# Kernel tuning notes

Measured on AMD Instinct MI355X. Metric: run time of the kernel, lower is better.

Reference implementation:

```python
import jax, jax.numpy as jnp
import numpy as np

C_IN = 256
K = 4
C_QK = C_IN // K  # 64


def setup_inputs() -> dict:
    key = jax.random.key(0)
    ks = jax.random.split(key, 9)
    B, C, H, W = 4, C_IN, 64, 64
    s = 0.02
    return {
        "x": jax.random.normal(ks[0], (B, C, H, W), dtype=jnp.float32),
        # 1x1 convs stored as dense [out, in] matrices (kernel_size=1)
        "wq": jax.random.normal(ks[1], (C_QK, C), dtype=jnp.float32) * s,
        "bq": jax.random.normal(ks[2], (C_QK,), dtype=jnp.float32) * s,
        "wk": jax.random.normal(ks[3], (C_QK, C), dtype=jnp.float32) * s,
        "bk": jax.random.normal(ks[4], (C_QK,), dtype=jnp.float32) * s,
        "wv": jax.random.normal(ks[5], (C, C), dtype=jnp.float32) * s,
        "bv": jax.random.normal(ks[6], (C,), dtype=jnp.float32) * s,
        "wg": jax.random.normal(ks[7], (C, C), dtype=jnp.float32) * s,
        "bg": jax.random.normal(ks[8], (C,), dtype=jnp.float32) * s,
    }


def reference(x, wq, bq, wk, bk, wv, bv, wg, bg):
    B, C, H, W = x.shape
    N = H * W
    xf = x.reshape(B, C, N)  # [B, C, N]
    # 1x1 conv == per-pixel linear over channels
    q = jnp.einsum("oc,bcn->bon", wq, xf) + bq[None, :, None]  # [B, Cqk, N]
    k = jnp.einsum("oc,bcn->bon", wk, xf) + bk[None, :, None]  # [B, Cqk, N]
    v = jnp.einsum("oc,bcn->bon", wv, xf) + bv[None, :, None]  # [B, C, N]
    # energy[b, n, m] = <q[:, n], k[:, m]>  (n = query pos, m = key pos)
    energy = jnp.einsum("bon,bom->bnm", q, k)  # [B, N, N]
    energy = jax.nn.elu(energy) / N
    # out[b, c, m] = sum_n v[b, c, n] * energy[b, n, m]
    out = jnp.einsum("bcn,bnm->bcm", v, energy).reshape(B, C, H, W)
    out = jnp.einsum("oc,bchw->bohw", wg, out) + bg[None, :, None, None]
    return out
```

## Files before the change

kernel.cpp:

```cpp
#include <hip/hip_runtime.h>

#define B_ 4
#define C_ 256
#define CQK 64
#define N_ 4096
#define SEG 2
#define SEGN (N_ / SEG)
#define NB 128
#define ITERS (SEGN / NB)
#define TS 512

typedef _Float16 f16;
typedef __attribute__((ext_vector_type(8))) _Float16 f16x8;
typedef __attribute__((ext_vector_type(4))) _Float16 f16x4;
typedef __attribute__((ext_vector_type(4))) float f32x4;
typedef __attribute__((ext_vector_type(4))) float float4v;

#define TILE_OFF(l15, quad) ((l15) * 32 + (quad) * 8)

__global__ __launch_bounds__(256) void prep_w(
    const float* __restrict__ wq, const float* __restrict__ wk,
    const float* __restrict__ wv, const float* __restrict__ wg,
    f16* __restrict__ WQt, f16* __restrict__ WKt, f16* __restrict__ WVt,
    f16* __restrict__ WGt) {
  int chunk = blockIdx.x * 256 + threadIdx.x;
  if (chunk >= 20480) return;
  const float* src;
  f16* dst;
  int lo;
  if (chunk < 2048) { src = wq; dst = WQt; lo = chunk * 8; }
  else if (chunk < 4096) { src = wk; dst = WKt; lo = (chunk - 2048) * 8; }
  else if (chunk < 12288) { src = wv; dst = WVt; lo = (chunk - 4096) * 8; }
  else { src = wg; dst = WGt; lo = (chunk - 12288) * 8; }
  int o = lo >> 8, k = lo & 255;
  f16x8 v;
#pragma unroll
  for (int j = 0; j < 8; j++) v[j] = (f16)src[lo + j];
  *(f16x8*)(dst + ((size_t)(o >> 4) * 8 + (k >> 5)) * TS + (o & 15) * 32 + (k & 31)) = v;
}

__global__ __launch_bounds__(256) void proj(
    const float* __restrict__ x, const f16* __restrict__ WQt,
    const f16* __restrict__ WKt, const f16* __restrict__ WVt,
    const float* __restrict__ bq, const float* __restrict__ bk,
    const float* __restrict__ bv, f16* __restrict__ QTt, f16* __restrict__ KTt,
    f16* __restrict__ Vt) {
  __shared__ float xs[32][265];
  __shared__ f16 xt[2 * 8 * TS];
  int n0 = blockIdx.x * 32;
  int b = blockIdx.y;
  int tid = threadIdx.x, lane = tid & 63, w = tid >> 6;
  int l15 = lane & 15, quad = lane >> 4;
  const float* xb = x + (size_t)b * C_ * N_;

#pragma unroll
  for (int i = 0; i < 8; i++) {
    int c = i * 32 + (tid >> 3);
    int n4 = (tid & 7) * 4;
    float4v f4 = *(const float4v*)(xb + (size_t)c * N_ + n0 + n4);
#pragma unroll
    for (int j = 0; j < 4; j++) xs[n4 + j][c] = f4[j];
  }
  __syncthreads();
#pragma unroll
  for (int i = 0; i < 4; i++) {
    int t = w + i * 4;
    int nt = t >> 3, kt = t & 7;
    f16x8 v;
#pragma unroll
    for (int j = 0; j < 8; j++)
      v[j] = (f16)xs[nt * 16 + l15][kt * 32 + quad * 8 + j];
    *(f16x8*)(xt + (nt * 8 + kt) * TS + l15 * 32 + quad * 8) = v;
  }
  __syncthreads();

  f32x4 acc[6][2];
#pragma unroll
  for (int j = 0; j < 6; j++)
#pragma unroll
    for (int nt = 0; nt < 2; nt++) acc[j][nt] = (f32x4){0.f, 0.f, 0.f, 0.f};

#pragma unroll
  for (int kt = 0; kt < 8; kt++) {
    f16x8 xf[2];
#pragma unroll
    for (int nt = 0; nt < 2; nt++)
      xf[nt] = *(const f16x8*)(xt + (nt * 8 + kt) * TS + TILE_OFF(l15, quad));
#pragma unroll
    for (int j = 0; j < 6; j++) {
      int g = w * 6 + j;
      const f16* Wt;
      int ot;
      bool isV = g < 16;
      if (isV) { Wt = WVt; ot = g; }
      else if (g < 20) { Wt = WQt; ot = g - 16; }
      else { Wt = WKt; ot = g - 20; }
      f16x8 wf = *(const f16x8*)(Wt + ((size_t)ot * 8 + kt) * TS + TILE_OFF(l15, quad));
#pragma unroll
      for (int nt = 0; nt < 2; nt++)
        acc[j][nt] = isV
            ? __builtin_amdgcn_mfma_f32_16x16x32_f16(xf[nt], wf, acc[j][nt], 0, 0, 0)
            : __builtin_amdgcn_mfma_f32_16x16x32_f16(wf, xf[nt], acc[j][nt], 0, 0, 0);
    }
  }

  f16* vbout = Vt + (size_t)b * C_ * N_;
#pragma unroll
  for (int j = 0; j < 6; j++) {
    int g = w * 6 + j;
    if (g < 16) {
      float bvv = bv[16 * g + l15];
#pragma unroll
      for (int nt = 0; nt < 2; nt++) {
        f16x4 vals;
#pragma unroll
        for (int r = 0; r < 4; r++) vals[r] = (f16)(acc[j][nt][r] + bvv);
        *(f16x4*)(vbout + ((size_t)g * 128 + (n0 >> 5)) * TS +
                  l15 * 32 + 16 * nt + 4 * quad) = vals;
      }
    } else {
      int oq = (g < 20) ? (g - 16) : (g - 20);
      const float* bias = (g < 20) ? bq : bk;
      f16* ob = ((g < 20) ? QTt : KTt) + (size_t)b * N_ * CQK;
#pragma unroll
      for (int nt = 0; nt < 2; nt++) {
        f16x4 vals;
#pragma unroll
        for (int r = 0; r < 4; r++)
          vals[r] = (f16)(acc[j][nt][r] + bias[16 * oq + 4 * quad + r]);
        *(f16x4*)(ob + (((size_t)(n0 >> 4) + nt) * 2 + (oq >> 1)) * TS + l15 * 32 +
                  16 * (oq & 1) + 4 * quad) = vals;
      }
    }
  }
}

__global__ __launch_bounds__(256, 2) void attn(const f16* __restrict__ qt,
                                               const f16* __restrict__ kt,
                                               const f16* __restrict__ v,
                                               const f16* __restrict__ WGt,
                                               f16* __restrict__ part) {
  __shared__ __align__(16) f16 sPt[2][64][128];
  int sb = blockIdx.x;
  int seg = sb >> 2;
  int b = sb & 3;
  int m0 = blockIdx.y * 64;
  int tid = threadIdx.x, lane = tid & 63, w = tid >> 6;
  int l15 = lane & 15, quad = lane >> 4;
  const f16* qtb = qt + (size_t)b * N_ * CQK;
  const f16* ktb = kt + (size_t)b * N_ * CQK;
  const f16* vb = v + (size_t)b * C_ * N_;

  f32x4 oacc[4][4];
#pragma unroll
  for (int ct = 0; ct < 4; ct++)
#pragma unroll
    for (int mt = 0; mt < 4; mt++) oacc[ct][mt] = (f32x4){0.f, 0.f, 0.f, 0.f};

  f16x8 kf[4][2];
#pragma unroll
  for (int mt = 0; mt < 4; mt++)
#pragma unroll
    for (int ks = 0; ks < 2; ks++)
      kf[mt][ks] = *(const f16x8*)(ktb + ((size_t)((m0 >> 4) + mt) * 2 + ks) * TS +
                                   TILE_OFF(l15, quad));

  f16x8 qf[2][2];
#pragma unroll
  for (int nt = 0; nt < 2; nt++)
#pragma unroll
    for (int ks = 0; ks < 2; ks++)
      qf[nt][ks] = *(const f16x8*)(qtb +
                                   ((size_t)(((seg * SEGN) >> 4) + 2 * w + nt) * 2 + ks) * TS +
                                   TILE_OFF(l15, quad));

  {
    char* buf = (char*)sPt[0];
#pragma unroll
    for (int nt = 0; nt < 2; nt++) {
      f32x4 sacc[4];
#pragma unroll
      for (int mt = 0; mt < 4; mt++) sacc[mt] = (f32x4){0.f, 0.f, 0.f, 0.f};
#pragma unroll
      for (int ks = 0; ks < 2; ks++)
#pragma unroll
        for (int mt = 0; mt < 4; mt++)
          sacc[mt] = __builtin_amdgcn_mfma_f32_16x16x32_f16(qf[nt][ks], kf[mt][ks],
                                                            sacc[mt], 0, 0, 0);
#pragma unroll
      for (int mt = 0; mt < 4; mt++) {
        f16x4 p;
#pragma unroll
        for (int r = 0; r < 4; r++) {
          float s = sacc[mt][r];
          p[r] = (f16)(s > 0.0f ? s : (__expf(s) - 1.0f));
        }
        int row = 16 * mt + l15;
        int colb = (64 * w + 32 * nt + 8 * quad) ^ ((row & 7) << 4);
        *(f16x4*)(buf + row * 256 + colb) = p;
      }
    }
  }
  {
    int nq = seg * SEGN + NB;
#pragma unroll
    for (int nt = 0; nt < 2; nt++)
#pragma unroll
      for (int ks = 0; ks < 2; ks++)
        qf[nt][ks] = *(const f16x8*)(qtb +
                                     ((size_t)((nq >> 4) + 2 * w + nt) * 2 + ks) * TS +
                                     TILE_OFF(l15, quad));
  }
  __syncthreads();

  for (int it = 0; it < ITERS; it++) {
    int n0 = seg * SEGN + it * NB;
    char* rbuf = (char*)sPt[it & 1];
    char* wbuf = (char*)sPt[(it + 1) & 1];
    bool hasNext = (it + 1 < ITERS);

    f16x8 vfA[2][4];
#pragma unroll
    for (int ks = 0; ks < 2; ks++)
#pragma unroll
      for (int ct = 0; ct < 4; ct++)
        vfA[ks][ct] = *(const f16x8*)(vb +
                                      ((size_t)(4 * w + ct) * 128 + (n0 >> 5) + ks) * TS +
                                      TILE_OFF(l15, quad));

    f32x4 s0[4], s1[4];
    if (hasNext) {
#pragma unroll
      for (int mt = 0; mt < 4; mt++) s0[mt] = (f32x4){0.f, 0.f, 0.f, 0.f};
#pragma unroll
      for (int ks = 0; ks < 2; ks++)
#pragma unroll
        for (int mt = 0; mt < 4; mt++)
          s0[mt] = __builtin_amdgcn_mfma_f32_16x16x32_f16(qf[0][ks], kf[mt][ks],
                                                          s0[mt], 0, 0, 0);
    }

    f16x8 pa[4];
#pragma unroll
    for (int mt = 0; mt < 4; mt++) {
      int row = 16 * mt + l15;
      pa[mt] = *(const f16x8*)(rbuf + row * 256 + ((quad * 16) ^ ((row & 7) << 4)));
    }
#pragma unroll
    for (int ct = 0; ct < 4; ct++)
#pragma unroll
      for (int mt = 0; mt < 4; mt++)
        oacc[ct][mt] = __builtin_amdgcn_mfma_f32_16x16x32_f16(vfA[0][ct], pa[mt],
                                                              oacc[ct][mt], 0, 0, 0);

    f16x8 vfB[2][4];
#pragma unroll
    for (int ks = 0; ks < 2; ks++)
#pragma unroll
      for (int ct = 0; ct < 4; ct++)
        vfB[ks][ct] = *(const f16x8*)(vb + ((size_t)(4 * w + ct) * 128 + (n0 >> 5) +
                                            2 + ks) * TS +
                                      TILE_OFF(l15, quad));

    if (hasNext) {
#pragma unroll
      for (int mt = 0; mt < 4; mt++) {
        f16x4 p;
#pragma unroll
        for (int r = 0; r < 4; r++) {
          float s = s0[mt][r];
          p[r] = (f16)(s > 0.0f ? s : (__expf(s) - 1.0f));
        }
        int row = 16 * mt + l15;
        int colb = (64 * w + 8 * quad) ^ ((row & 7) << 4);
        *(f16x4*)(wbuf + row * 256 + colb) = p;
      }
    }

#pragma unroll
    for (int mt = 0; mt < 4; mt++) {
      int row = 16 * mt + l15;
      pa[mt] = *(const f16x8*)(rbuf + row * 256 + ((64 + quad * 16) ^ ((row & 7) << 4)));
    }
#pragma unroll
    for (int ct = 0; ct < 4; ct++)
#pragma unroll
      for (int mt = 0; mt < 4; mt++)
        oacc[ct][mt] = __builtin_amdgcn_mfma_f32_16x16x32_f16(vfA[1][ct], pa[mt],
                                                              oacc[ct][mt], 0, 0, 0);

    if (hasNext) {
#pragma unroll
      for (int mt = 0; mt < 4; mt++) s1[mt] = (f32x4){0.f, 0.f, 0.f, 0.f};
#pragma unroll
      for (int ks = 0; ks < 2; ks++)
#pragma unroll
        for (int mt = 0; mt < 4; mt++)
          s1[mt] = __builtin_amdgcn_mfma_f32_16x16x32_f16(qf[1][ks], kf[mt][ks],
                                                          s1[mt], 0, 0, 0);
    }

#pragma unroll
    for (int mt = 0; mt < 4; mt++) {
      int row = 16 * mt + l15;
      pa[mt] = *(const f16x8*)(rbuf + row * 256 + ((128 + quad * 16) ^ ((row & 7) << 4)));
    }
#pragma unroll
    for (int ct = 0; ct < 4; ct++)
#pragma unroll
      for (int mt = 0; mt < 4; mt++)
        oacc[ct][mt] = __builtin_amdgcn_mfma_f32_16x16x32_f16(vfB[0][ct], pa[mt],
                                                              oacc[ct][mt], 0, 0, 0);

    if (hasNext) {
#pragma unroll
      for (int mt = 0; mt < 4; mt++) {
        f16x4 p;
#pragma unroll
        for (int r = 0; r < 4; r++) {
          float s = s1[mt][r];
          p[r] = (f16)(s > 0.0f ? s : (__expf(s) - 1.0f));
        }
        int row = 16 * mt + l15;
        int colb = (64 * w + 32 + 8 * quad) ^ ((row & 7) << 4);
        *(f16x4*)(wbuf + row * 256 + colb) = p;
      }
      if (it + 2 < ITERS) {
        int nq = seg * SEGN + (it + 2) * NB;
#pragma unroll
        for (int nt = 0; nt < 2; nt++)
#pragma unroll
          for (int ks = 0; ks < 2; ks++)
            qf[nt][ks] = *(const f16x8*)(qtb +
                                         ((size_t)((nq >> 4) + 2 * w + nt) * 2 + ks) * TS +
                                         TILE_OFF(l15, quad));
      }
    }

#pragma unroll
    for (int mt = 0; mt < 4; mt++) {
      int row = 16 * mt + l15;
      pa[mt] = *(const f16x8*)(rbuf + row * 256 + ((192 + quad * 16) ^ ((row & 7) << 4)));
    }
#pragma unroll
    for (int ct = 0; ct < 4; ct++)
#pragma unroll
      for (int mt = 0; mt < 4; mt++)
        oacc[ct][mt] = __builtin_amdgcn_mfma_f32_16x16x32_f16(vfB[1][ct], pa[mt],
                                                              oacc[ct][mt], 0, 0, 0);

    __syncthreads();
  }

  f16* obuf = (f16*)sPt;
#pragma unroll
  for (int ct = 0; ct < 4; ct++) {
#pragma unroll
    for (int mt = 0; mt < 4; mt++) {
      f16x4 vals;
#pragma unroll
      for (int r = 0; r < 4; r++)
        vals[r] = (f16)(oacc[ct][mt][r] * (1.0f / (float)N_));
      *(f16x4*)(obuf + (mt * 8 + 2 * w + (ct >> 1)) * TS + l15 * 32 +
                16 * (ct & 1) + 4 * quad) = vals;
    }
  }
  __syncthreads();
  f32x4 accO[4][4];
#pragma unroll
  for (int ot = 0; ot < 4; ot++)
#pragma unroll
    for (int mt = 0; mt < 4; mt++) accO[ot][mt] = (f32x4){0.f, 0.f, 0.f, 0.f};
#pragma unroll
  for (int kt = 0; kt < 8; kt++) {
    f16x8 bO[4];
#pragma unroll
    for (int mt = 0; mt < 4; mt++)
      bO[mt] = *(const f16x8*)(obuf + (mt * 8 + kt) * TS + TILE_OFF(l15, quad));
#pragma unroll
    for (int ot = 0; ot < 4; ot++) {
      f16x8 af = *(const f16x8*)(WGt + ((size_t)(4 * w + ot) * 8 + kt) * TS +
                                 TILE_OFF(l15, quad));
#pragma unroll
      for (int mt = 0; mt < 4; mt++)
        accO[ot][mt] = __builtin_amdgcn_mfma_f32_16x16x32_f16(af, bO[mt], accO[ot][mt], 0, 0, 0);
    }
  }
  f16* pb = part + ((size_t)(seg * B_ + b) * C_) * N_;
#pragma unroll
  for (int ot = 0; ot < 4; ot++) {
#pragma unroll
    for (int mt = 0; mt < 4; mt++) {
      int m = m0 + 16 * mt + l15;
#pragma unroll
      for (int r = 0; r < 4; r++) {
        int o = 64 * w + 16 * ot + 4 * quad + r;
        pb[(size_t)o * N_ + m] = (f16)accO[ot][mt][r];
      }
    }
  }
}

__global__ __launch_bounds__(256) void combine(const f16* __restrict__ part,
                                               const float* __restrict__ bg,
                                               float* __restrict__ out) {
  size_t i = ((size_t)blockIdx.x * 256 + threadIdx.x) * 8;
  f16x8 p0 = *(const f16x8*)(part + i);
  f16x8 p1 = *(const f16x8*)(part + (size_t)B_ * C_ * N_ + i);
  float bgo = bg[(i >> 12) & 255];
  float4v r0, r1;
#pragma unroll
  for (int j = 0; j < 4; j++) r0[j] = (float)p0[j] + (float)p1[j] + bgo;
#pragma unroll
  for (int j = 0; j < 4; j++) r1[j] = (float)p0[4 + j] + (float)p1[4 + j] + bgo;
  *(float4v*)(out + i) = r0;
  *(float4v*)(out + i + 4) = r1;
}

extern "C" void kernel_launch(void* const* d_in, const int* in_sizes, int n_in,
                              void* d_out, int out_size, void* d_ws, size_t ws_size,
                              hipStream_t stream) {
  const float* x = (const float*)d_in[0];
  const float* wq = (const float*)d_in[1];
  const float* bq = (const float*)d_in[2];
  const float* wk = (const float*)d_in[3];
  const float* bk = (const float*)d_in[4];
  const float* wv = (const float*)d_in[5];
  const float* bv = (const float*)d_in[6];
  const float* wg = (const float*)d_in[7];
  const float* bg = (const float*)d_in[8];
  float* out = (float*)d_out;

  char* ws = (char*)d_ws;
  f16* QTt = (f16*)ws; ws += (size_t)B_ * N_ * CQK * sizeof(f16);
  f16* KTt = (f16*)ws; ws += (size_t)B_ * N_ * CQK * sizeof(f16);
  f16* Vt  = (f16*)ws; ws += (size_t)B_ * C_ * N_ * sizeof(f16);
  f16* WQt = (f16*)ws; ws += (size_t)CQK * C_ * sizeof(f16);
  f16* WKt = (f16*)ws; ws += (size_t)CQK * C_ * sizeof(f16);
  f16* WVt = (f16*)ws; ws += (size_t)C_ * C_ * sizeof(f16);
  f16* WGt = (f16*)ws; ws += (size_t)C_ * C_ * sizeof(f16);
  f16* PART = (f16*)ws; ws += (size_t)SEG * B_ * C_ * N_ * sizeof(f16);

  prep_w<<<dim3(80), 256, 0, stream>>>(wq, wk, wv, wg, WQt, WKt, WVt, WGt);
  proj<<<dim3(N_ / 32, B_), 256, 0, stream>>>(x, WQt, WKt, WVt, bq, bk, bv,
                                              QTt, KTt, Vt);
  attn<<<dim3(SEG * B_, N_ / 64), 256, 0, stream>>>(QTt, KTt, Vt, WGt, PART);
  combine<<<dim3(2048), 256, 0, stream>>>(PART, bg, out);
}
```

Baseline: 161.0 us.

## Fuse four kernels into one persistent kernel with software grid barriers

```diff
diff --git a/kernel.cpp b/kernel.cpp
--- a/kernel.cpp
+++ b/kernel.cpp
@@ -9,6 +9,7 @@
 #define NB 128
 #define ITERS (SEGN / NB)
 #define TS 512
+#define NBLK 512
 
 typedef _Float16 f16;
 typedef __attribute__((ext_vector_type(8))) _Float16 f16x8;
@@ -18,403 +19,425 @@
 
 #define TILE_OFF(l15, quad) ((l15) * 32 + (quad) * 8)
 
-__global__ __launch_bounds__(256) void prep_w(
-    const float* __restrict__ wq, const float* __restrict__ wk,
-    const float* __restrict__ wv, const float* __restrict__ wg,
-    f16* __restrict__ WQt, f16* __restrict__ WKt, f16* __restrict__ WVt,
-    f16* __restrict__ WGt) {
-  int chunk = blockIdx.x * 256 + threadIdx.x;
-  if (chunk >= 20480) return;
-  const float* src;
-  f16* dst;
-  int lo;
-  if (chunk < 2048) { src = wq; dst = WQt; lo = chunk * 8; }
-  else if (chunk < 4096) { src = wk; dst = WKt; lo = (chunk - 2048) * 8; }
-  else if (chunk < 12288) { src = wv; dst = WVt; lo = (chunk - 4096) * 8; }
-  else { src = wg; dst = WGt; lo = (chunk - 12288) * 8; }
-  int o = lo >> 8, k = lo & 255;
-  f16x8 v;
-#pragma unroll
-  for (int j = 0; j < 8; j++) v[j] = (f16)src[lo + j];
-  *(f16x8*)(dst + ((size_t)(o >> 4) * 8 + (k >> 5)) * TS + (o & 15) * 32 + (k & 31)) = v;
+__device__ __forceinline__ void gridbar(unsigned* bar) {
+  __syncthreads();
+  if (threadIdx.x == 0) {
+    __threadfence();
+    unsigned gen = __hip_atomic_load(bar + 1, __ATOMIC_RELAXED, __HIP_MEMORY_SCOPE_AGENT);
+    unsigned old = atomicAdd(bar, 1u);
+    if (old == NBLK - 1) {
+      __hip_atomic_store(bar, 0u, __ATOMIC_RELAXED, __HIP_MEMORY_SCOPE_AGENT);
+      __hip_atomic_fetch_add(bar + 1, 1u, __ATOMIC_RELEASE, __HIP_MEMORY_SCOPE_AGENT);
+    } else {
+      while (__hip_atomic_load(bar + 1, __ATOMIC_ACQUIRE, __HIP_MEMORY_SCOPE_AGENT) == gen)
+        __builtin_amdgcn_s_sleep(2);
+    }
+    __threadfence();
+  }
+  __syncthreads();
 }
 
-__global__ __launch_bounds__(256) void proj(
-    const float* __restrict__ x, const f16* __restrict__ WQt,
-    const f16* __restrict__ WKt, const f16* __restrict__ WVt,
-    const float* __restrict__ bq, const float* __restrict__ bk,
-    const float* __restrict__ bv, f16* __restrict__ QTt, f16* __restrict__ KTt,
-    f16* __restrict__ Vt) {
-  __shared__ float xs[32][265];
-  __shared__ f16 xt[2 * 8 * TS];
-  int n0 = blockIdx.x * 32;
-  int b = blockIdx.y;
+__global__ __launch_bounds__(256, 2) void fused(
+    const float* __restrict__ x, const float* __restrict__ wq,
+    const float* __restrict__ bq, const float* __restrict__ wk,
+    const float* __restrict__ bk, const float* __restrict__ wv,
+    const float* __restrict__ bv, const float* __restrict__ wg,
+    const float* __restrict__ bg, f16* __restrict__ QTt, f16* __restrict__ KTt,
+    f16* __restrict__ Vt, f16* __restrict__ WQt, f16* __restrict__ WKt,
+    f16* __restrict__ WVt, f16* __restrict__ WGt, f16* __restrict__ part,
+    float* __restrict__ out, unsigned* __restrict__ bar) {
+  __shared__ __align__(16) union {
+    struct { float xs[32][265]; f16 xt[2 * 8 * TS]; } p;
+    f16 sPt[2][64][128];
+  } sh;
+  int bid = blockIdx.x;
   int tid = threadIdx.x, lane = tid & 63, w = tid >> 6;
   int l15 = lane & 15, quad = lane >> 4;
-  const float* xb = x + (size_t)b * C_ * N_;
-
-#pragma unroll
-  for (int i = 0; i < 8; i++) {
-    int c = i * 32 + (tid >> 3);
-    int n4 = (tid & 7) * 4;
-    float4v f4 = *(const float4v*)(xb + (size_t)c * N_ + n0 + n4);
-#pragma unroll
-    for (int j = 0; j < 4; j++) xs[n4 + j][c] = f4[j];
+
+  {
+    int chunk = bid * 256 + tid;
+    if (chunk < 20480) {
+      const float* src;
+      f16* dst;
+      int lo;
+      if (chunk < 2048) { src = wq; dst = WQt; lo = chunk * 8; }
+      else if (chunk < 4096) { src = wk; dst = WKt; lo = (chunk - 2048) * 8; }
+      else if (chunk < 12288) { src = wv; dst = WVt; lo = (chunk - 4096) * 8; }
+      else { src = wg; dst = WGt; lo = (chunk - 12288) * 8; }
+      int o = lo >> 8, k = lo & 255;
+      f16x8 v;
+#pragma unroll
+      for (int j = 0; j < 8; j++) v[j] = (f16)src[lo + j];
+      *(f16x8*)(dst + ((size_t)(o >> 4) * 8 + (k >> 5)) * TS + (o & 15) * 32 +
+                (k & 31)) = v;
+    }
   }
-  __syncthreads();
-#pragma unroll
-  for (int i = 0; i < 4; i++) {
-    int t = w + i * 4;
-    int nt = t >> 3, kt = t & 7;
-    f16x8 v;
-#pragma unroll
-    for (int j = 0; j < 8; j++)
-      v[j] = (f16)xs[nt * 16 + l15][kt * 32 + quad * 8 + j];
-    *(f16x8*)(xt + (nt * 8 + kt) * TS + l15 * 32 + quad * 8) = v;
-  }
-  __syncthreads();
-
-  f32x4 acc[6][2];
-#pragma unroll
-  for (int j = 0; j < 6; j++)
-#pragma unroll
-    for (int nt = 0; nt < 2; nt++) acc[j][nt] = (f32x4){0.f, 0.f, 0.f, 0.f};
-
-#pragma unroll
-  for (int kt = 0; kt < 8; kt++) {
-    f16x8 xf[2];
-#pragma unroll
-    for (int nt = 0; nt < 2; nt++)
-      xf[nt] = *(const f16x8*)(xt + (nt * 8 + kt) * TS + TILE_OFF(l15, quad));
+  gridbar(bar);
+
+  {
+    int n0 = (bid & 127) * 32;
+    int b = bid >> 7;
+    const float* xb = x + (size_t)b * C_ * N_;
+
+#pragma unroll
+    for (int i = 0; i < 8; i++) {
+      int c = i * 32 + (tid >> 3);
+      int n4 = (tid & 7) * 4;
+      float4v f4 = *(const float4v*)(xb + (size_t)c * N_ + n0 + n4);
+#pragma unroll
+      for (int j = 0; j < 4; j++) sh.p.xs[n4 + j][c] = f4[j];
+    }
+    __syncthreads();
+#pragma unroll
+    for (int i = 0; i < 4; i++) {
+      int t = w + i * 4;
+      int nt = t >> 3, kt = t & 7;
+      f16x8 v;
+#pragma unroll
+      for (int j = 0; j < 8; j++)
+        v[j] = (f16)sh.p.xs[nt * 16 + l15][kt * 32 + quad * 8 + j];
+      *(f16x8*)(sh.p.xt + (nt * 8 + kt) * TS + l15 * 32 + quad * 8) = v;
+    }
+    __syncthreads();
+
+    f32x4 acc[6][2];
+#pragma unroll
+    for (int j = 0; j < 6; j++)
+#pragma unroll
+      for (int nt = 0; nt < 2; nt++) acc[j][nt] = (f32x4){0.f, 0.f, 0.f, 0.f};
+
+#pragma unroll
+    for (int kt = 0; kt < 8; kt++) {
+      f16x8 xf[2];
+#pragma unroll
+      for (int nt = 0; nt < 2; nt++)
+        xf[nt] = *(const f16x8*)(sh.p.xt + (nt * 8 + kt) * TS + TILE_OFF(l15, quad));
+#pragma unroll
+      for (int j = 0; j < 6; j++) {
+        int g = w * 6 + j;
+        const f16* Wt;
+        int ot;
+        bool isV = g < 16;
+        if (isV) { Wt = WVt; ot = g; }
+        else if (g < 20) { Wt = WQt; ot = g - 16; }
+        else { Wt = WKt; ot = g - 20; }
+        f16x8 wf = *(const f16x8*)(Wt + ((size_t)ot * 8 + kt) * TS + TILE_OFF(l15, quad));
+#pragma unroll
+        for (int nt = 0; nt < 2; nt++)
+          acc[j][nt] = isV
+              ? __builtin_amdgcn_mfma_f32_16x16x32_f16(xf[nt], wf, acc[j][nt], 0, 0, 0)
+              : __builtin_amdgcn_mfma_f32_16x16x32_f16(wf, xf[nt], acc[j][nt], 0, 0, 0);
+      }
+    }
+
+    f16* vbout = Vt + (size_t)b * C_ * N_;
 #pragma unroll
     for (int j = 0; j < 6; j++) {
       int g = w * 6 + j;
-      const f16* Wt;
-      int ot;
-      bool isV = g < 16;
-      if (isV) { Wt = WVt; ot = g; }
-      else if (g < 20) { Wt = WQt; ot = g - 16; }
-      else { Wt = WKt; ot = g - 20; }
-      f16x8 wf = *(const f16x8*)(Wt + ((size_t)ot * 8 + kt) * TS + TILE_OFF(l15, quad));
-#pragma unroll
-      for (int nt = 0; nt < 2; nt++)
-        acc[j][nt] = isV
-            ? __builtin_amdgcn_mfma_f32_16x16x32_f16(xf[nt], wf, acc[j][nt], 0, 0, 0)
-            : __builtin_amdgcn_mfma_f32_16x16x32_f16(wf, xf[nt], acc[j][nt], 0, 0, 0);
+      if (g < 16) {
+        float bvv = bv[16 * g + l15];
+#pragma unroll
+        for (int nt = 0; nt < 2; nt++) {
+          f16x4 vals;
+#pragma unroll
+          for (int r = 0; r < 4; r++) vals[r] = (f16)(acc[j][nt][r] + bvv);
+          *(f16x4*)(vbout + ((size_t)g * 128 + (n0 >> 5)) * TS +
+                    l15 * 32 + 16 * nt + 4 * quad) = vals;
+        }
+      } else {
+        int oq = (g < 20) ? (g - 16) : (g - 20);
+        const float* bias = (g < 20) ? bq : bk;
+        f16* ob = ((g < 20) ? QTt : KTt) + (size_t)b * N_ * CQK;
+#pragma unroll
+        for (int nt = 0; nt < 2; nt++) {
+          f16x4 vals;
+#pragma unroll
+          for (int r = 0; r < 4; r++)
+            vals[r] = (f16)(acc[j][nt][r] + bias[16 * oq + 4 * quad + r]);
+          *(f16x4*)(ob + (((size_t)(n0 >> 4) + nt) * 2 + (oq >> 1)) * TS + l15 * 32 +
+                    16 * (oq & 1) + 4 * quad) = vals;
+        }
+      }
     }
   }
-
-  f16* vbout = Vt + (size_t)b * C_ * N_;
-#pragma unroll
-  for (int j = 0; j < 6; j++) {
-    int g = w * 6 + j;
-    if (g < 16) {
-      float bvv = bv[16 * g + l15];
-#pragma unroll
-      for (int nt = 0; nt < 2; nt++) {
-        f16x4 vals;
-#pragma unroll
-        for (int r = 0; r < 4; r++) vals[r] = (f16)(acc[j][nt][r] + bvv);
-        *(f16x4*)(vbout + ((size_t)g * 128 + (n0 >> 5)) * TS +
-                  l15 * 32 + 16 * nt + 4 * quad) = vals;
-      }
-    } else {
-      int oq = (g < 20) ? (g - 16) : (g - 20);
-      const float* bias = (g < 20) ? bq : bk;
-      f16* ob = ((g < 20) ? QTt : KTt) + (size_t)b * N_ * CQK;
-#pragma unroll
-      for (int nt = 0; nt < 2; nt++) {
-        f16x4 vals;
-#pragma unroll
-        for (int r = 0; r < 4; r++)
-          vals[r] = (f16)(acc[j][nt][r] + bias[16 * oq + 4 * quad + r]);
-        *(f16x4*)(ob + (((size_t)(n0 >> 4) + nt) * 2 + (oq >> 1)) * TS + l15 * 32 +
-                  16 * (oq & 1) + 4 * quad) = vals;
-      }
-    }
-  }
-}
-
-__global__ __launch_bounds__(256, 2) void attn(const f16* __restrict__ qt,
-                                               const f16* __restrict__ kt,
-                                               const f16* __restrict__ v,
-                                               const f16* __restrict__ WGt,
-                                               f16* __restrict__ part) {
-  __shared__ __align__(16) f16 sPt[2][64][128];
-  int sb = blockIdx.x;
-  int seg = sb >> 2;
-  int b = sb & 3;
-  int m0 = blockIdx.y * 64;
-  int tid = threadIdx.x, lane = tid & 63, w = tid >> 6;
-  int l15 = lane & 15, quad = lane >> 4;
-  const f16* qtb = qt + (size_t)b * N_ * CQK;
-  const f16* ktb = kt + (size_t)b * N_ * CQK;
-  const f16* vb = v + (size_t)b * C_ * N_;
-
-  f32x4 oacc[4][4];
-#pragma unroll
-  for (int ct = 0; ct < 4; ct++)
-#pragma unroll
-    for (int mt = 0; mt < 4; mt++) oacc[ct][mt] = (f32x4){0.f, 0.f, 0.f, 0.f};
-
-  f16x8 kf[4][2];
-#pragma unroll
-  for (int mt = 0; mt < 4; mt++)
-#pragma unroll
-    for (int ks = 0; ks < 2; ks++)
-      kf[mt][ks] = *(const f16x8*)(ktb + ((size_t)((m0 >> 4) + mt) * 2 + ks) * TS +
-                                   TILE_OFF(l15, quad));
-
-  f16x8 qf[2][2];
-#pragma unroll
-  for (int nt = 0; nt < 2; nt++)
-#pragma unroll
-    for (int ks = 0; ks < 2; ks++)
-      qf[nt][ks] = *(const f16x8*)(qtb +
-                                   ((size_t)(((seg * SEGN) >> 4) + 2 * w + nt) * 2 + ks) * TS +
-                                   TILE_OFF(l15, quad));
+  gridbar(bar);
 
   {
-    char* buf = (char*)sPt[0];
-#pragma unroll
-    for (int nt = 0; nt < 2; nt++) {
-      f32x4 sacc[4];
-#pragma unroll
-      for (int mt = 0; mt < 4; mt++) sacc[mt] = (f32x4){0.f, 0.f, 0.f, 0.f};
+    int sb = bid & 7;
+    int seg = sb >> 2;
+    int b = sb & 3;
+    int m0 = (bid >> 3) * 64;
+    const f16* qtb = QTt + (size_t)b * N_ * CQK;
+    const f16* ktb = KTt + (size_t)b * N_ * CQK;
+    const f16* vb = Vt + (size_t)b * C_ * N_;
+
+    f32x4 oacc[4][4];
+#pragma unroll
+    for (int ct = 0; ct < 4; ct++)
+#pragma unroll
+      for (int mt = 0; mt < 4; mt++) oacc[ct][mt] = (f32x4){0.f, 0.f, 0.f, 0.f};
+
+    f16x8 kf[4][2];
+#pragma unroll
+    for (int mt = 0; mt < 4; mt++)
 #pragma unroll
       for (int ks = 0; ks < 2; ks++)
-#pragma unroll
-        for (int mt = 0; mt < 4; mt++)
-          sacc[mt] = __builtin_amdgcn_mfma_f32_16x16x32_f16(qf[nt][ks], kf[mt][ks],
-                                                            sacc[mt], 0, 0, 0);
-#pragma unroll
-      for (int mt = 0; mt < 4; mt++) {
-        f16x4 p;
-#pragma unroll
-        for (int r = 0; r < 4; r++) {
-          float s = sacc[mt][r];
-          p[r] = (f16)(s > 0.0f ? s : (__expf(s) - 1.0f));
-        }
-        int row = 16 * mt + l15;
-        int colb = (64 * w + 32 * nt + 8 * quad) ^ ((row & 7) << 4);
-        *(f16x4*)(buf + row * 256 + colb) = p;
-      }
-    }
-  }
-  {
-    int nq = seg * SEGN + NB;
+        kf[mt][ks] = *(const f16x8*)(ktb + ((size_t)((m0 >> 4) + mt) * 2 + ks) * TS +
+                                     TILE_OFF(l15, quad));
+
+    f16x8 qf[2][2];
 #pragma unroll
     for (int nt = 0; nt < 2; nt++)
 #pragma unroll
       for (int ks = 0; ks < 2; ks++)
         qf[nt][ks] = *(const f16x8*)(qtb +
-                                     ((size_t)((nq >> 4) + 2 * w + nt) * 2 + ks) * TS +
+                                     ((size_t)(((seg * SEGN) >> 4) + 2 * w + nt) * 2 + ks) * TS +
                                      TILE_OFF(l15, quad));
+
+    {
+      char* buf = (char*)sh.sPt[0];
+#pragma unroll
+      for (int nt = 0; nt < 2; nt++) {
+        f32x4 sacc[4];
+#pragma unroll
+        for (int mt = 0; mt < 4; mt++) sacc[mt] = (f32x4){0.f, 0.f, 0.f, 0.f};
+#pragma unroll
+        for (int ks = 0; ks < 2; ks++)
+#pragma unroll
+          for (int mt = 0; mt < 4; mt++)
+            sacc[mt] = __builtin_amdgcn_mfma_f32_16x16x32_f16(qf[nt][ks], kf[mt][ks],
+                                                              sacc[mt], 0, 0, 0);
+#pragma unroll
+        for (int mt = 0; mt < 4; mt++) {
+          f16x4 p;
+#pragma unroll
+          for (int r = 0; r < 4; r++) {
+            float s = sacc[mt][r];
+            p[r] = (f16)(s > 0.0f ? s : (__expf(s) - 1.0f));
+          }
+          int row = 16 * mt + l15;
+          int colb = (64 * w + 32 * nt + 8 * quad) ^ ((row & 7) << 4);
+          *(f16x4*)(buf + row * 256 + colb) = p;
+        }
+      }
+    }
+    {
+      int nq = seg * SEGN + NB;
+#pragma unroll
+      for (int nt = 0; nt < 2; nt++)
+#pragma unroll
+        for (int ks = 0; ks < 2; ks++)
+          qf[nt][ks] = *(const f16x8*)(qtb +
+                                       ((size_t)((nq >> 4) + 2 * w + nt) * 2 + ks) * TS +
+                                       TILE_OFF(l15, quad));
+    }
+    __syncthreads();
+
+    for (int it = 0; it < ITERS; it++) {
+      int n0 = seg * SEGN + it * NB;
+      char* rbuf = (char*)sh.sPt[it & 1];
+      char* wbuf = (char*)sh.sPt[(it + 1) & 1];
+      bool hasNext = (it + 1 < ITERS);
+
+      f16x8 vfA[2][4];
+#pragma unroll
+      for (int ks = 0; ks < 2; ks++)
+#pragma unroll
+        for (int ct = 0; ct < 4; ct++)
+          vfA[ks][ct] = *(const f16x8*)(vb +
+                                        ((size_t)(4 * w + ct) * 128 + (n0 >> 5) + ks) * TS +
+                                        TILE_OFF(l15, quad));
+
+      f32x4 s0[4], s1[4];
+      if (hasNext) {
+#pragma unroll
+        for (int mt = 0; mt < 4; mt++) s0[mt] = (f32x4){0.f, 0.f, 0.f, 0.f};
+#pragma unroll
+        for (int ks = 0; ks < 2; ks++)
+#pragma unroll
+          for (int mt = 0; mt < 4; mt++)
+            s0[mt] = __builtin_amdgcn_mfma_f32_16x16x32_f16(qf[0][ks], kf[mt][ks],
+                                                            s0[mt], 0, 0, 0);
+      }
+
+      f16x8 pa[4];
+#pragma unroll
+      for (int mt = 0; mt < 4; mt++) {
+        int row = 16 * mt + l15;
+        pa[mt] = *(const f16x8*)(rbuf + row * 256 + ((quad * 16) ^ ((row & 7) << 4)));
+      }
+#pragma unroll
+      for (int ct = 0; ct < 4; ct++)
+#pragma unroll
+        for (int mt = 0; mt < 4; mt++)
+          oacc[ct][mt] = __builtin_amdgcn_mfma_f32_16x16x32_f16(vfA[0][ct], pa[mt],
+                                                                oacc[ct][mt], 0, 0, 0);
+
+      f16x8 vfB[2][4];
+#pragma unroll
+      for (int ks = 0; ks < 2; ks++)
+#pragma unroll
+        for (int ct = 0; ct < 4; ct++)
+          vfB[ks][ct] = *(const f16x8*)(vb + ((size_t)(4 * w + ct) * 128 + (n0 >> 5) +
+                                              2 + ks) * TS +
+                                        TILE_OFF(l15, quad));
+
+      if (hasNext) {
+#pragma unroll
+        for (int mt = 0; mt < 4; mt++) {
+          f16x4 p;
+#pragma unroll
+          for (int r = 0; r < 4; r++) {
+            float s = s0[mt][r];
+            p[r] = (f16)(s > 0.0f ? s : (__expf(s) - 1.0f));
+          }
+          int row = 16 * mt + l15;
+          int colb = (64 * w + 8 * quad) ^ ((row & 7) << 4);
+          *(f16x4*)(wbuf + row * 256 + colb) = p;
+        }
+      }
+
+#pragma unroll
+      for (int mt = 0; mt < 4; mt++) {
+        int row = 16 * mt + l15;
+        pa[mt] = *(const f16x8*)(rbuf + row * 256 + ((64 + quad * 16) ^ ((row & 7) << 4)));
+      }
+#pragma unroll
+      for (int ct = 0; ct < 4; ct++)
+#pragma unroll
+        for (int mt = 0; mt < 4; mt++)
+          oacc[ct][mt] = __builtin_amdgcn_mfma_f32_16x16x32_f16(vfA[1][ct], pa[mt],
+                                                                oacc[ct][mt], 0, 0, 0);
+
+      if (hasNext) {
+#pragma unroll
+        for (int mt = 0; mt < 4; mt++) s1[mt] = (f32x4){0.f, 0.f, 0.f, 0.f};
+#pragma unroll
+        for (int ks = 0; ks < 2; ks++)
+#pragma unroll
+          for (int mt = 0; mt < 4; mt++)
+            s1[mt] = __builtin_amdgcn_mfma_f32_16x16x32_f16(qf[1][ks], kf[mt][ks],
+                                                            s1[mt], 0, 0, 0);
+      }
+
+#pragma unroll
+      for (int mt = 0; mt < 4; mt++) {
+        int row = 16 * mt + l15;
+        pa[mt] = *(const f16x8*)(rbuf + row * 256 + ((128 + quad * 16) ^ ((row & 7) << 4)));
+      }
+#pragma unroll
+      for (int ct = 0; ct < 4; ct++)
+#pragma unroll
+        for (int mt = 0; mt < 4; mt++)
+          oacc[ct][mt] = __builtin_amdgcn_mfma_f32_16x16x32_f16(vfB[0][ct], pa[mt],
+                                                                oacc[ct][mt], 0, 0, 0);
+
+      if (hasNext) {
+#pragma unroll
+        for (int mt = 0; mt < 4; mt++) {
+          f16x4 p;
+#pragma unroll
+          for (int r = 0; r < 4; r++) {
+            float s = s1[mt][r];
+            p[r] = (f16)(s > 0.0f ? s : (__expf(s) - 1.0f));
+          }
+          int row = 16 * mt + l15;
+          int colb = (64 * w + 32 + 8 * quad) ^ ((row & 7) << 4);
+          *(f16x4*)(wbuf + row * 256 + colb) = p;
+        }
+        if (it + 2 < ITERS) {
+          int nq = seg * SEGN + (it + 2) * NB;
+#pragma unroll
+          for (int nt = 0; nt < 2; nt++)
+#pragma unroll
+            for (int ks = 0; ks < 2; ks++)
+              qf[nt][ks] = *(const f16x8*)(qtb +
+                                           ((size_t)((nq >> 4) + 2 * w + nt) * 2 + ks) * TS +
+                                           TILE_OFF(l15, quad));
+        }
+      }
+
+#pragma unroll
+      for (int mt = 0; mt < 4; mt++) {
+        int row = 16 * mt + l15;
+        pa[mt] = *(const f16x8*)(rbuf + row * 256 + ((192 + quad * 16) ^ ((row & 7) << 4)));
+      }
+#pragma unroll
+      for (int ct = 0; ct < 4; ct++)
+#pragma unroll
+        for (int mt = 0; mt < 4; mt++)
+          oacc[ct][mt] = __builtin_amdgcn_mfma_f32_16x16x32_f16(vfB[1][ct], pa[mt],
+                                                                oacc[ct][mt], 0, 0, 0);
+
+      __syncthreads();
+    }
+
+    f16* obuf = (f16*)sh.sPt;
+#pragma unroll
+    for (int ct = 0; ct < 4; ct++) {
+#pragma unroll
+      for (int mt = 0; mt < 4; mt++) {
+        f16x4 vals;
+#pragma unroll
+        for (int r = 0; r < 4; r++)
+          vals[r] = (f16)(oacc[ct][mt][r] * (1.0f / (float)N_));
+        *(f16x4*)(obuf + (mt * 8 + 2 * w + (ct >> 1)) * TS + l15 * 32 +
+                  16 * (ct & 1) + 4 * quad) = vals;
+      }
+    }
+    __syncthreads();
+    f32x4 accO[4][4];
+#pragma unroll
+    for (int ot = 0; ot < 4; ot++)
+#pragma unroll
+      for (int mt = 0; mt < 4; mt++) accO[ot][mt] = (f32x4){0.f, 0.f, 0.f, 0.f};
+#pragma unroll
+    for (int kt = 0; kt < 8; kt++) {
+      f16x8 bO[4];
+#pragma unroll
+      for (int mt = 0; mt < 4; mt++)
+        bO[mt] = *(const f16x8*)(obuf + (mt * 8 + kt) * TS + TILE_OFF(l15, quad));
+#pragma unroll
+      for (int ot = 0; ot < 4; ot++) {
+        f16x8 af = *(const f16x8*)(WGt + ((size_t)(4 * w + ot) * 8 + kt) * TS +
+                                   TILE_OFF(l15, quad));
+#pragma unroll
+        for (int mt = 0; mt < 4; mt++)
+          accO[ot][mt] = __builtin_amdgcn_mfma_f32_16x16x32_f16(af, bO[mt], accO[ot][mt],
+                                                                0, 0, 0);
+      }
+    }
+    f16* pb = part + ((size_t)(seg * B_ + b) * C_) * N_;
+#pragma unroll
+    for (int ot = 0; ot < 4; ot++) {
+#pragma unroll
+      for (int mt = 0; mt < 4; mt++) {
+        int m = m0 + 16 * mt + l15;
+#pragma unroll
+        for (int r = 0; r < 4; r++) {
+          int o = 64 * w + 16 * ot + 4 * quad + r;
+          pb[(size_t)o * N_ + m] = (f16)accO[ot][mt][r];
+        }
+      }
+    }
   }
-  __syncthreads();
-
-  for (int it = 0; it < ITERS; it++) {
-    int n0 = seg * SEGN + it * NB;
-    char* rbuf = (char*)sPt[it & 1];
-    char* wbuf = (char*)sPt[(it + 1) & 1];
-    bool hasNext = (it + 1 < ITERS);
-
-    f16x8 vfA[2][4];
-#pragma unroll
-    for (int ks = 0; ks < 2; ks++)
-#pragma unroll
-      for (int ct = 0; ct < 4; ct++)
-        vfA[ks][ct] = *(const f16x8*)(vb +
-                                      ((size_t)(4 * w + ct) * 128 + (n0 >> 5) + ks) * TS +
-                                      TILE_OFF(l15, quad));
-
-    f32x4 s0[4], s1[4];
-    if (hasNext) {
-#pragma unroll
-      for (int mt = 0; mt < 4; mt++) s0[mt] = (f32x4){0.f, 0.f, 0.f, 0.f};
-#pragma unroll
-      for (int ks = 0; ks < 2; ks++)
-#pragma unroll
-        for (int mt = 0; mt < 4; mt++)
-          s0[mt] = __builtin_amdgcn_mfma_f32_16x16x32_f16(qf[0][ks], kf[mt][ks],
-                                                          s0[mt], 0, 0, 0);
-    }
-
-    f16x8 pa[4];
-#pragma unroll
-    for (int mt = 0; mt < 4; mt++) {
-      int row = 16 * mt + l15;
-      pa[mt] = *(const f16x8*)(rbuf + row * 256 + ((quad * 16) ^ ((row & 7) << 4)));
-    }
-#pragma unroll
-    for (int ct = 0; ct < 4; ct++)
-#pragma unroll
-      for (int mt = 0; mt < 4; mt++)
-        oacc[ct][mt] = __builtin_amdgcn_mfma_f32_16x16x32_f16(vfA[0][ct], pa[mt],
-                                                              oacc[ct][mt], 0, 0, 0);
-
-    f16x8 vfB[2][4];
-#pragma unroll
-    for (int ks = 0; ks < 2; ks++)
-#pragma unroll
-      for (int ct = 0; ct < 4; ct++)
-        vfB[ks][ct] = *(const f16x8*)(vb + ((size_t)(4 * w + ct) * 128 + (n0 >> 5) +
-                                            2 + ks) * TS +
-                                      TILE_OFF(l15, quad));
-
-    if (hasNext) {
-#pragma unroll
-      for (int mt = 0; mt < 4; mt++) {
-        f16x4 p;
-#pragma unroll
-        for (int r = 0; r < 4; r++) {
-          float s = s0[mt][r];
-          p[r] = (f16)(s > 0.0f ? s : (__expf(s) - 1.0f));
-        }
-        int row = 16 * mt + l15;
-        int colb = (64 * w + 8 * quad) ^ ((row & 7) << 4);
-        *(f16x4*)(wbuf + row * 256 + colb) = p;
-      }
-    }
-
-#pragma unroll
-    for (int mt = 0; mt < 4; mt++) {
-      int row = 16 * mt + l15;
-      pa[mt] = *(const f16x8*)(rbuf + row * 256 + ((64 + quad * 16) ^ ((row & 7) << 4)));
-    }
-#pragma unroll
-    for (int ct = 0; ct < 4; ct++)
-#pragma unroll
-      for (int mt = 0; mt < 4; mt++)
-        oacc[ct][mt] = __builtin_amdgcn_mfma_f32_16x16x32_f16(vfA[1][ct], pa[mt],
-                                                              oacc[ct][mt], 0, 0, 0);
-
-    if (hasNext) {
-#pragma unroll
-      for (int mt = 0; mt < 4; mt++) s1[mt] = (f32x4){0.f, 0.f, 0.f, 0.f};
-#pragma unroll
-      for (int ks = 0; ks < 2; ks++)
-#pragma unroll
-        for (int mt = 0; mt < 4; mt++)
-          s1[mt] = __builtin_amdgcn_mfma_f32_16x16x32_f16(qf[1][ks], kf[mt][ks],
-                                                          s1[mt], 0, 0, 0);
-    }
-
-#pragma unroll
-    for (int mt = 0; mt < 4; mt++) {
-      int row = 16 * mt + l15;
-      pa[mt] = *(const f16x8*)(rbuf + row * 256 + ((128 + quad * 16) ^ ((row & 7) << 4)));
-    }
-#pragma unroll
-    for (int ct = 0; ct < 4; ct++)
-#pragma unroll
-      for (int mt = 0; mt < 4; mt++)
-        oacc[ct][mt] = __builtin_amdgcn_mfma_f32_16x16x32_f16(vfB[0][ct], pa[mt],
-                                                              oacc[ct][mt], 0, 0, 0);
-
-    if (hasNext) {
-#pragma unroll
-      for (int mt = 0; mt < 4; mt++) {
-        f16x4 p;
-#pragma unroll
-        for (int r = 0; r < 4; r++) {
-          float s = s1[mt][r];
-          p[r] = (f16)(s > 0.0f ? s : (__expf(s) - 1.0f));
-        }
-        int row = 16 * mt + l15;
-        int colb = (64 * w + 32 + 8 * quad) ^ ((row & 7) << 4);
-        *(f16x4*)(wbuf + row * 256 + colb) = p;
-      }
-      if (it + 2 < ITERS) {
-        int nq = seg * SEGN + (it + 2) * NB;
-#pragma unroll
-        for (int nt = 0; nt < 2; nt++)
-#pragma unroll
-          for (int ks = 0; ks < 2; ks++)
-            qf[nt][ks] = *(const f16x8*)(qtb +
-                                         ((size_t)((nq >> 4) + 2 * w + nt) * 2 + ks) * TS +
-                                         TILE_OFF(l15, quad));
-      }
-    }
-
-#pragma unroll
-    for (int mt = 0; mt < 4; mt++) {
-      int row = 16 * mt + l15;
-      pa[mt] = *(const f16x8*)(rbuf + row * 256 + ((192 + quad * 16) ^ ((row & 7) << 4)));
-    }
-#pragma unroll
-    for (int ct = 0; ct < 4; ct++)
-#pragma unroll
-      for (int mt = 0; mt < 4; mt++)
-        oacc[ct][mt] = __builtin_amdgcn_mfma_f32_16x16x32_f16(vfB[1][ct], pa[mt],
-                                                              oacc[ct][mt], 0, 0, 0);
-
-    __syncthreads();
+  gridbar(bar);
+
+  {
+    for (int r = 0; r < 4; r++) {
+      size_t i = (((size_t)r * NBLK + bid) * 256 + tid) * 8;
+      f16x8 p0 = *(const f16x8*)(part + i);
+      f16x8 p1 = *(const f16x8*)(part + (size_t)B_ * C_ * N_ + i);
+      float bgo = bg[(i >> 12) & 255];
+      float4v r0, r1;
+#pragma unroll
+      for (int j = 0; j < 4; j++) r0[j] = (float)p0[j] + (float)p1[j] + bgo;
+#pragma unroll
+      for (int j = 0; j < 4; j++) r1[j] = (float)p0[4 + j] + (float)p1[4 + j] + bgo;
+      *(float4v*)(out + i) = r0;
+      *(float4v*)(out + i + 4) = r1;
+    }
   }
-
-  f16* obuf = (f16*)sPt;
-#pragma unroll
-  for (int ct = 0; ct < 4; ct++) {
-#pragma unroll
-    for (int mt = 0; mt < 4; mt++) {
-      f16x4 vals;
-#pragma unroll
-      for (int r = 0; r < 4; r++)
-        vals[r] = (f16)(oacc[ct][mt][r] * (1.0f / (float)N_));
-      *(f16x4*)(obuf + (mt * 8 + 2 * w + (ct >> 1)) * TS + l15 * 32 +
-                16 * (ct & 1) + 4 * quad) = vals;
-    }
-  }
-  __syncthreads();
-  f32x4 accO[4][4];
-#pragma unroll
-  for (int ot = 0; ot < 4; ot++)
-#pragma unroll
-    for (int mt = 0; mt < 4; mt++) accO[ot][mt] = (f32x4){0.f, 0.f, 0.f, 0.f};
-#pragma unroll
-  for (int kt = 0; kt < 8; kt++) {
-    f16x8 bO[4];
-#pragma unroll
-    for (int mt = 0; mt < 4; mt++)
-      bO[mt] = *(const f16x8*)(obuf + (mt * 8 + kt) * TS + TILE_OFF(l15, quad));
-#pragma unroll
-    for (int ot = 0; ot < 4; ot++) {
-      f16x8 af = *(const f16x8*)(WGt + ((size_t)(4 * w + ot) * 8 + kt) * TS +
-                                 TILE_OFF(l15, quad));
-#pragma unroll
-      for (int mt = 0; mt < 4; mt++)
-        accO[ot][mt] = __builtin_amdgcn_mfma_f32_16x16x32_f16(af, bO[mt], accO[ot][mt], 0, 0, 0);
-    }
-  }
-  f16* pb = part + ((size_t)(seg * B_ + b) * C_) * N_;
-#pragma unroll
-  for (int ot = 0; ot < 4; ot++) {
-#pragma unroll
-    for (int mt = 0; mt < 4; mt++) {
-      int m = m0 + 16 * mt + l15;
-#pragma unroll
-      for (int r = 0; r < 4; r++) {
-        int o = 64 * w + 16 * ot + 4 * quad + r;
-        pb[(size_t)o * N_ + m] = (f16)accO[ot][mt][r];
-      }
-    }
-  }
-}
-
-__global__ __launch_bounds__(256) void combine(const f16* __restrict__ part,
-                                               const float* __restrict__ bg,
-                                               float* __restrict__ out) {
-  size_t i = ((size_t)blockIdx.x * 256 + threadIdx.x) * 8;
-  f16x8 p0 = *(const f16x8*)(part + i);
-  f16x8 p1 = *(const f16x8*)(part + (size_t)B_ * C_ * N_ + i);
-  float bgo = bg[(i >> 12) & 255];
-  float4v r0, r1;
-#pragma unroll
-  for (int j = 0; j < 4; j++) r0[j] = (float)p0[j] + (float)p1[j] + bgo;
-#pragma unroll
-  for (int j = 0; j < 4; j++) r1[j] = (float)p0[4 + j] + (float)p1[4 + j] + bgo;
-  *(float4v*)(out + i) = r0;
-  *(float4v*)(out + i + 4) = r1;
 }
 
 extern "C" void kernel_launch(void* const* d_in, const int* in_sizes, int n_in,
@@ -432,6 +455,7 @@
   float* out = (float*)d_out;
 
   char* ws = (char*)d_ws;
+  unsigned* bar = (unsigned*)ws; ws += 64;
   f16* QTt = (f16*)ws; ws += (size_t)B_ * N_ * CQK * sizeof(f16);
   f16* KTt = (f16*)ws; ws += (size_t)B_ * N_ * CQK * sizeof(f16);
   f16* Vt  = (f16*)ws; ws += (size_t)B_ * C_ * N_ * sizeof(f16);
@@ -441,9 +465,8 @@
   f16* WGt = (f16*)ws; ws += (size_t)C_ * C_ * sizeof(f16);
   f16* PART = (f16*)ws; ws += (size_t)SEG * B_ * C_ * N_ * sizeof(f16);
 
-  prep_w<<<dim3(80), 256, 0, stream>>>(wq, wk, wv, wg, WQt, WKt, WVt, WGt);
-  proj<<<dim3(N_ / 32, B_), 256, 0, stream>>>(x, WQt, WKt, WVt, bq, bk, bv,
-                                              QTt, KTt, Vt);
-  attn<<<dim3(SEG * B_, N_ / 64), 256, 0, stream>>>(QTt, KTt, Vt, WGt, PART);
-  combine<<<dim3(2048), 256, 0, stream>>>(PART, bg, out);
+  hipMemsetAsync(bar, 0, 64, stream);
+  fused<<<dim3(NBLK), 256, 0, stream>>>(x, wq, bq, wk, bk, wv, bv, wg, bg,
+                                        QTt, KTt, Vt, WQt, WKt, WVt, WGt,
+                                        PART, out, bar);
 }
```

Result: slower. 399.9 us (+148.4%).
